# Kernel tuning notes

Measured on AMD Instinct MI355X. Metric: run time of the kernel, lower is better.

The kernel has to match this reference:

```python
import jax, jax.numpy as jnp
import numpy as np

FEAT = 1152
HID = [768, 512, 256]
WS = 32
LN_EPS = 1e-5


def _ln(x, g, b):
    mu = jnp.mean(x, axis=-1, keepdims=True)
    var = jnp.mean(jnp.square(x - mu), axis=-1, keepdims=True)
    return (x - mu) * jax.lax.rsqrt(var + LN_EPS) * g + b


def setup_inputs() -> dict:
    key = jax.random.key(0)
    ks = jax.random.split(key, 16)
    B, N, C = 8, 9216, FEAT

    def lin(k, din, dout):
        s = 1.0 / np.sqrt(din)
        k1, k2 = jax.random.split(k)
        return (jax.random.uniform(k1, (din, dout), jnp.float32, -s, s),
                jax.random.uniform(k2, (dout,), jnp.float32, -s, s))

    x = jax.random.normal(ks[0], (B, N, C), jnp.float32)
    W1, b1 = lin(ks[1], C, HID[0])
    W2, b2 = lin(ks[2], HID[0], HID[1])
    W3, b3 = lin(ks[3], HID[1], HID[2])
    Wo, bo = lin(ks[4], HID[2], C)
    red = C // 8
    ca_w1, ca_b1 = lin(ks[5], C, red)
    ca_w2, ca_b2 = lin(ks[6], red, C)
    return {
        "x": x,
        "W1": W1, "b1": b1, "g1": jnp.ones((HID[0],)), "be1": jnp.zeros((HID[0],)),
        "W2": W2, "b2": b2, "g2": jnp.ones((HID[1],)), "be2": jnp.zeros((HID[1],)),
        "W3": W3, "b3": b3, "g3": jnp.ones((HID[2],)), "be3": jnp.zeros((HID[2],)),
        "Wo": Wo, "bo": bo,
        "ca_w1": ca_w1, "ca_b1": ca_b1, "ca_w2": ca_w2, "ca_b2": ca_b2,
    }


def reference(x, W1, b1, g1, be1, W2, b2, g2, be2, W3, b3, g3, be3,
              Wo, bo, ca_w1, ca_b1, ca_w2, ca_b2):
    B, N, C = x.shape
    # projection + hidden blocks: Linear -> GELU(exact) -> LayerNorm
    h = _ln(jax.nn.gelu(x @ W1 + b1, approximate=False), g1, be1)
    h = _ln(jax.nn.gelu(h @ W2 + b2, approximate=False), g2, be2)
    h = _ln(jax.nn.gelu(h @ W3 + b3, approximate=False), g3, be3)
    y = h @ Wo + bo  # (B, N, C)
    # SE channel attention: global avg-pool over seq, 1x1 convs (=linear)
    pooled = jnp.mean(y, axis=1)                                  # (B, C)
    s = jax.nn.relu(pooled @ ca_w1 + ca_b1)                       # (B, C/8)
    s = jax.nn.sigmoid(s @ ca_w2 + ca_b2)                         # (B, C)
    y = y * s[:, None, :]
    # block-diagonal local self-attention, window = WS, scale 1/sqrt(C)
    nw = N // WS
    yw = y.reshape(B, nw, WS, C)
    scores = jnp.einsum('bwqc,bwkc->bwqk', yw, yw) / jnp.sqrt(jnp.asarray(C, y.dtype))
    attn = jax.nn.softmax(scores, axis=-1)
    out = jnp.einsum('bwqk,bwkc->bwqc', attn, yw)
    return out.reshape(B, N, C)
```

## Files before the change

kernel.cpp:

```cpp
#include <hip/hip_runtime.h>
#include <cstdint>
#include <cstddef>

typedef __bf16 bf16;
typedef __bf16 bf16x8 __attribute__((ext_vector_type(8)));
typedef float f32x4 __attribute__((ext_vector_type(4)));

__device__ __forceinline__ void gload_lds16(const bf16* g, bf16* l) {
    __builtin_amdgcn_global_load_lds((const __attribute__((address_space(1))) void*)g,
                                     (__attribute__((address_space(3))) void*)l, 16, 0, 0);
}

__global__ void cvt_f32_bf16_kernel(const float* __restrict__ in, bf16* __restrict__ outp, size_t n) {
    const size_t i = ((size_t)blockIdx.x * 256 + threadIdx.x) * 8;
    if (i >= n) return;
    const float4 a = *(const float4*)(in + i);
    const float4 b = *(const float4*)(in + i + 4);
    bf16x8 o;
    o[0] = (bf16)a.x; o[1] = (bf16)a.y; o[2] = (bf16)a.z; o[3] = (bf16)a.w;
    o[4] = (bf16)b.x; o[5] = (bf16)b.y; o[6] = (bf16)b.z; o[7] = (bf16)b.w;
    *(bf16x8*)(outp + i) = o;
}

__global__ void wtrans_kernel(const float* __restrict__ W, bf16* __restrict__ Wt, int K, int N) {
    const int idx = blockIdx.x * 256 + threadIdx.x;
    const int n = idx / K, k = idx - n * K;
    Wt[idx] = (bf16)W[(size_t)k * N + n];
}

__global__ void gemm_bf16_kernel(const bf16* __restrict__ A, const bf16* __restrict__ Bt,
                                 const float* __restrict__ bias, bf16* __restrict__ C,
                                 int K, int N, int do_gelu)
{
    __shared__ bf16 Alds[128 * 64];
    __shared__ bf16 Blds[128 * 64];
    const int t = threadIdx.x;
    const int w = t >> 6;
    const int l = t & 63;
    const int l15 = l & 15, l4 = l >> 4;
    const int m0 = blockIdx.y << 7;
    const int n0 = blockIdx.x << 7;
    const int wm = (w >> 1) << 6;
    const int wn = (w & 1) << 6;

    f32x4 acc[4][4] = {};

    int sr[4], sg[4];
#pragma unroll
    for (int i = 0; i < 4; ++i) {
        const int flat = i * 256 + t;
        sr[i] = flat >> 3;
        sg[i] = ((flat & 7) ^ (sr[i] & 7)) << 3;
    }

    for (int k0 = 0; k0 < K; k0 += 64) {
#pragma unroll
        for (int i = 0; i < 4; ++i) {
            gload_lds16(A + (size_t)(m0 + sr[i]) * K + (k0 + sg[i]),
                        &Alds[(size_t)(i * 256 + (w << 6)) << 3]);
            gload_lds16(Bt + (size_t)(n0 + sr[i]) * K + (k0 + sg[i]),
                        &Blds[(size_t)(i * 256 + (w << 6)) << 3]);
        }
        __syncthreads();
#pragma unroll
        for (int kk = 0; kk < 2; ++kk) {
            bf16x8 af[4], bfv[4];
#pragma unroll
            for (int i = 0; i < 4; ++i) {
                const int r = wm + (i << 4) + l15;
                const int g = (kk << 2) + l4;
                af[i] = *(const bf16x8*)&Alds[(r << 6) + ((g ^ (r & 7)) << 3)];
                const int rn = wn + (i << 4) + l15;
                bfv[i] = *(const bf16x8*)&Blds[(rn << 6) + ((g ^ (rn & 7)) << 3)];
            }
#pragma unroll
            for (int i = 0; i < 4; ++i)
#pragma unroll
                for (int j = 0; j < 4; ++j)
                    acc[i][j] = __builtin_amdgcn_mfma_f32_16x16x32_bf16(af[i], bfv[j], acc[i][j], 0, 0, 0);
        }
        __syncthreads();
    }

#pragma unroll
    for (int i = 0; i < 4; ++i) {
        const int mb = m0 + wm + (i << 4) + (l4 << 2);
#pragma unroll
        for (int j = 0; j < 4; ++j) {
            const int col = n0 + wn + (j << 4) + l15;
            const float bv = bias[col];
#pragma unroll
            for (int r = 0; r < 4; ++r) {
                float v = acc[i][j][r] + bv;
                if (do_gelu) v = 0.5f * v * (1.0f + erff(v * 0.70710678118654752f));
                C[(size_t)(mb + r) * N + col] = (bf16)v;
            }
        }
    }
}

template <int N>
__global__ void ln_kernel(bf16* __restrict__ H, const float* __restrict__ g,
                          const float* __restrict__ be)
{
    constexpr int NG = N / 8;
    const int t = threadIdx.x;
    bf16* hp = H + (size_t)blockIdx.x * N;
    float v[8];
    float s1 = 0.f, s2 = 0.f;
    if (t < NG) {
        const bf16x8 hv = *(const bf16x8*)(hp + t * 8);
#pragma unroll
        for (int e = 0; e < 8; ++e) { v[e] = (float)hv[e]; s1 += v[e]; s2 += v[e] * v[e]; }
    }
#pragma unroll
    for (int m = 1; m < 64; m <<= 1) { s1 += __shfl_xor(s1, m, 64); s2 += __shfl_xor(s2, m, 64); }
    __shared__ float red[4];
    const int w = t >> 6;
    if ((t & 63) == 0) { red[w] = s1; red[w + 2] = s2; }
    __syncthreads();
    s1 = red[0] + red[1];
    s2 = red[2] + red[3];
    const float mu = s1 * (1.0f / N);
    const float rstd = rsqrtf(s2 * (1.0f / N) - mu * mu + 1e-5f);
    if (t < NG) {
        const float4 g0 = *(const float4*)(g + t * 8);
        const float4 g1 = *(const float4*)(g + t * 8 + 4);
        const float4 b0 = *(const float4*)(be + t * 8);
        const float4 b1 = *(const float4*)(be + t * 8 + 4);
        bf16x8 o;
        o[0] = (bf16)((v[0] - mu) * rstd * g0.x + b0.x);
        o[1] = (bf16)((v[1] - mu) * rstd * g0.y + b0.y);
        o[2] = (bf16)((v[2] - mu) * rstd * g0.z + b0.z);
        o[3] = (bf16)((v[3] - mu) * rstd * g0.w + b0.w);
        o[4] = (bf16)((v[4] - mu) * rstd * g1.x + b1.x);
        o[5] = (bf16)((v[5] - mu) * rstd * g1.y + b1.y);
        o[6] = (bf16)((v[6] - mu) * rstd * g1.z + b1.z);
        o[7] = (bf16)((v[7] - mu) * rstd * g1.w + b1.w);
        *(bf16x8*)(hp + t * 8) = o;
    }
}

__global__ void pool1_kernel(const bf16* __restrict__ Y, float* __restrict__ ppart) {
    const int c = blockIdx.x * 128 + threadIdx.x;
    const int nc = blockIdx.y;
    const int b = blockIdx.z;
    const bf16* yp = Y + ((size_t)b * 9216 + (size_t)nc * 256) * 1152 + c;
    float s = 0.f;
#pragma unroll 4
    for (int i = 0; i < 256; ++i) s += (float)yp[(size_t)i * 1152];
    ppart[((size_t)b * 36 + nc) * 1152 + c] = s;
}

__global__ void pool2_kernel(const float* __restrict__ ppart, float* __restrict__ pooled) {
    const int i = blockIdx.x * 256 + threadIdx.x;
    const int b = i / 1152, c = i - b * 1152;
    float s = 0.f;
#pragma unroll
    for (int j = 0; j < 36; ++j) s += ppart[((size_t)b * 36 + j) * 1152 + c];
    pooled[i] = s;
}

__global__ void se_kernel(const float* __restrict__ pooled,
                          const float* __restrict__ w1, const float* __restrict__ b1,
                          const float* __restrict__ w2, const float* __restrict__ b2,
                          float* __restrict__ sbuf)
{
    const int b = blockIdx.x, t = threadIdx.x;
    __shared__ float p[1152];
    __shared__ float t1[144];
    for (int c = t; c < 1152; c += 256) p[c] = pooled[b * 1152 + c] * (1.0f / 9216.0f);
    __syncthreads();
    if (t < 144) {
        float a = b1[t];
        for (int k = 0; k < 1152; ++k) a += p[k] * w1[k * 144 + t];
        t1[t] = a > 0.f ? a : 0.f;
    }
    __syncthreads();
    for (int c = t; c < 1152; c += 256) {
        float a = b2[c];
#pragma unroll 8
        for (int k = 0; k < 144; ++k) a += t1[k] * w2[k * 1152 + c];
        sbuf[b * 1152 + c] = 1.0f / (1.0f + expf(-a));
    }
}

__global__ void attn_kernel(const bf16* __restrict__ Y, const float* __restrict__ sbuf,
                            float* __restrict__ out)
{
    __shared__ bf16 yw[32 * 384];
    __shared__ float Sp[4][32][33];
    __shared__ bf16 P[32 * 32];

    const int t = threadIdx.x;
    const int w = t >> 6, l = t & 63;
    const int l15 = l & 15, l4 = l >> 4;
    const int wdx = blockIdx.x, b = blockIdx.y;

    const bf16* Yp = Y + ((size_t)b * 9216 + (size_t)wdx * 32) * 1152;
    const float* sv = sbuf + b * 1152;
    float* op = out + ((size_t)b * 9216 + (size_t)wdx * 32) * 1152;

    auto stage_chunk = [&](int cc) {
#pragma unroll
        for (int i = 0; i < 6; ++i) {
            const int flat = i * 256 + t;
            const int r = flat / 48;
            const int gg = flat - r * 48;
            const int c0 = cc * 384 + gg * 8;
            const bf16x8 yv = *(const bf16x8*)(Yp + (size_t)r * 1152 + c0);
            const float4 sa = *(const float4*)(sv + c0);
            const float4 sb = *(const float4*)(sv + c0 + 4);
            bf16x8 ov;
            ov[0] = (bf16)((float)yv[0] * sa.x);
            ov[1] = (bf16)((float)yv[1] * sa.y);
            ov[2] = (bf16)((float)yv[2] * sa.z);
            ov[3] = (bf16)((float)yv[3] * sa.w);
            ov[4] = (bf16)((float)yv[4] * sb.x);
            ov[5] = (bf16)((float)yv[5] * sb.y);
            ov[6] = (bf16)((float)yv[6] * sb.z);
            ov[7] = (bf16)((float)yv[7] * sb.w);
            *(bf16x8*)&yw[((r * 48) + (gg ^ (r & 7))) << 3] = ov;
        }
    };

    f32x4 acc[2][2] = {};
    for (int cc = 0; cc < 3; ++cc) {
        if (cc) __syncthreads();
        stage_chunk(cc);
        __syncthreads();
#pragma unroll
        for (int kkl = 0; kkl < 3; ++kkl) {
            const int g = ((w * 3 + kkl) << 2) + l4;
            bf16x8 af[2];
#pragma unroll
            for (int i = 0; i < 2; ++i) {
                const int r = (i << 4) + l15;
                af[i] = *(const bf16x8*)&yw[((r * 48) + (g ^ (r & 7))) << 3];
            }
#pragma unroll
            for (int i = 0; i < 2; ++i)
#pragma unroll
                for (int j = 0; j < 2; ++j)
                    acc[i][j] = __builtin_amdgcn_mfma_f32_16x16x32_bf16(af[i], af[j], acc[i][j], 0, 0, 0);
        }
    }
#pragma unroll
    for (int i = 0; i < 2; ++i)
#pragma unroll
        for (int j = 0; j < 2; ++j)
#pragma unroll
            for (int r = 0; r < 4; ++r)
                Sp[w][(i << 4) + (l4 << 2) + r][(j << 4) + l15] = acc[i][j][r];
    __syncthreads();

    {
        const int q = t >> 3, u = t & 7;
        float v[4];
#pragma unroll
        for (int e = 0; e < 4; ++e) {
            const int k2 = (u << 2) + e;
            v[e] = (Sp[0][q][k2] + Sp[1][q][k2] + Sp[2][q][k2] + Sp[3][q][k2]) * 0.029462782549439483f;
        }
        float mx = fmaxf(fmaxf(v[0], v[1]), fmaxf(v[2], v[3]));
#pragma unroll
        for (int m = 1; m < 8; m <<= 1) mx = fmaxf(mx, __shfl_xor(mx, m, 64));
        float sm = 0.f;
#pragma unroll
        for (int e = 0; e < 4; ++e) { v[e] = expf(v[e] - mx); sm += v[e]; }
#pragma unroll
        for (int m = 1; m < 8; m <<= 1) sm += __shfl_xor(sm, m, 64);
        const float inv = 1.0f / sm;
#pragma unroll
        for (int e = 0; e < 4; ++e) P[(q << 5) + (u << 2) + e] = (bf16)(v[e] * inv);
    }
    __syncthreads();

    bf16x8 pa[2];
#pragma unroll
    for (int i = 0; i < 2; ++i)
        pa[i] = *(const bf16x8*)&P[(((i << 4) + l15) << 5) + (l4 << 3)];

    for (int ci = 0; ci < 3; ++ci) {
        const int cc = (ci == 0) ? 2 : (ci - 1);
        if (ci) {
            __syncthreads();
            stage_chunk(cc);
            __syncthreads();
        }
        f32x4 pacc[2][6] = {};
#pragma unroll
        for (int jn = 0; jn < 6; ++jn) {
            const int nl = w * 96 + (jn << 4) + l15;
            const int gg = nl >> 3, e = nl & 7;
            bf16x8 bv;
#pragma unroll
            for (int j = 0; j < 8; ++j) {
                const int kr = (l4 << 3) + j;
                bv[j] = yw[(((kr * 48) + (gg ^ (kr & 7))) << 3) + e];
            }
#pragma unroll
            for (int i = 0; i < 2; ++i)
                pacc[i][jn] = __builtin_amdgcn_mfma_f32_16x16x32_bf16(pa[i], bv, pacc[i][jn], 0, 0, 0);
        }
#pragma unroll
        for (int i = 0; i < 2; ++i) {
            const int mb = (i << 4) + (l4 << 2);
#pragma unroll
            for (int jn = 0; jn < 6; ++jn) {
                const int cg = cc * 384 + w * 96 + (jn << 4) + l15;
#pragma unroll
                for (int r = 0; r < 4; ++r)
                    op[(size_t)(mb + r) * 1152 + cg] = pacc[i][jn][r];
            }
        }
    }
}

extern "C" void kernel_launch(void* const* d_in, const int* in_sizes, int n_in,
                              void* d_out, int out_size, void* d_ws, size_t ws_size,
                              hipStream_t stream)
{
    const float* x   = (const float*)d_in[0];
    const float* W1  = (const float*)d_in[1];
    const float* b1  = (const float*)d_in[2];
    const float* g1  = (const float*)d_in[3];
    const float* be1 = (const float*)d_in[4];
    const float* W2  = (const float*)d_in[5];
    const float* b2  = (const float*)d_in[6];
    const float* g2  = (const float*)d_in[7];
    const float* be2 = (const float*)d_in[8];
    const float* W3  = (const float*)d_in[9];
    const float* b3  = (const float*)d_in[10];
    const float* g3  = (const float*)d_in[11];
    const float* be3 = (const float*)d_in[12];
    const float* Wo  = (const float*)d_in[13];
    const float* bo  = (const float*)d_in[14];
    const float* cw1 = (const float*)d_in[15];
    const float* cb1 = (const float*)d_in[16];
    const float* cw2 = (const float*)d_in[17];
    const float* cb2 = (const float*)d_in[18];
    float* out = (float*)d_out;

    const int M = 8 * 9216;
    size_t off = 0;
    auto alloc = [&](size_t nbytes) {
        void* p = (char*)d_ws + off;
        off += (nbytes + 255) & ~(size_t)255;
        return p;
    };
    bf16* Xb  = (bf16*)alloc((size_t)M * 1152 * 2);
    bf16* Hb  = (bf16*)alloc((size_t)M * 768 * 2);
    bf16* H2  = (bf16*)alloc((size_t)M * 512 * 2);
    bf16* Wt1 = (bf16*)alloc(768ull * 1152 * 2);
    bf16* Wt2 = (bf16*)alloc(512ull * 768 * 2);
    bf16* Wt3 = (bf16*)alloc(256ull * 512 * 2);
    bf16* Wto = (bf16*)alloc(1152ull * 256 * 2);
    float* ppart  = (float*)alloc(8ull * 36 * 1152 * 4);
    float* pooled = (float*)alloc(8ull * 1152 * 4);
    float* sbuf   = (float*)alloc(8ull * 1152 * 4);
    bf16* H1 = Hb;
    bf16* H3 = Hb;
    bf16* Y  = Xb;

    cvt_f32_bf16_kernel<<<41472, 256, 0, stream>>>(x, Xb, (size_t)M * 1152);
    wtrans_kernel<<<3456, 256, 0, stream>>>(W1, Wt1, 1152, 768);
    wtrans_kernel<<<1536, 256, 0, stream>>>(W2, Wt2, 768, 512);
    wtrans_kernel<<<512,  256, 0, stream>>>(W3, Wt3, 512, 256);
    wtrans_kernel<<<1152, 256, 0, stream>>>(Wo, Wto, 256, 1152);

    gemm_bf16_kernel<<<dim3(6, 576), 256, 0, stream>>>(Xb, Wt1, b1, H1, 1152, 768, 1);
    ln_kernel<768><<<M, 128, 0, stream>>>(H1, g1, be1);
    gemm_bf16_kernel<<<dim3(4, 576), 256, 0, stream>>>(H1, Wt2, b2, H2, 768, 512, 1);
    ln_kernel<512><<<M, 128, 0, stream>>>(H2, g2, be2);
    gemm_bf16_kernel<<<dim3(2, 576), 256, 0, stream>>>(H2, Wt3, b3, H3, 512, 256, 1);
    ln_kernel<256><<<M, 128, 0, stream>>>(H3, g3, be3);
    gemm_bf16_kernel<<<dim3(9, 576), 256, 0, stream>>>(H3, Wto, bo, Y, 256, 1152, 0);

    pool1_kernel<<<dim3(9, 36, 8), 128, 0, stream>>>(Y, ppart);
    pool2_kernel<<<36, 256, 0, stream>>>(ppart, pooled);
    se_kernel<<<8, 256, 0, stream>>>(pooled, cw1, cb1, cw2, cb2, sbuf);
    attn_kernel<<<dim3(288, 8), 256, 0, stream>>>(Y, sbuf, out);
}
```

Before: 922.3 us.

## Fuse fp32-to-bf16 input conversion into first GEMM, swizzle blocks across XCDs, pack LN rows

Removes the standalone fp32→bf16 conversion pass over the input. The first GEMM now loads fp32 tiles of x straight into LDS and converts them to bf16 while building MFMA fragments, which avoids a full write and re-read of a large intermediate. The GEMM grids become 1-D with an XCD-aware block swizzle to improve L2 locality. The LayerNorm kernels now put several rows in each block to cut the number of launched blocks and idle threads. In exchange, the first GEMM uses twice the LDS for its A tile and does the conversion inside its inner loop.

```diff
diff --git a/kernel.cpp b/kernel.cpp
--- a/kernel.cpp
+++ b/kernel.cpp
@@ -10,16 +10,9 @@
     __builtin_amdgcn_global_load_lds((const __attribute__((address_space(1))) void*)g,
                                      (__attribute__((address_space(3))) void*)l, 16, 0, 0);
 }
-
-__global__ void cvt_f32_bf16_kernel(const float* __restrict__ in, bf16* __restrict__ outp, size_t n) {
-    const size_t i = ((size_t)blockIdx.x * 256 + threadIdx.x) * 8;
-    if (i >= n) return;
-    const float4 a = *(const float4*)(in + i);
-    const float4 b = *(const float4*)(in + i + 4);
-    bf16x8 o;
-    o[0] = (bf16)a.x; o[1] = (bf16)a.y; o[2] = (bf16)a.z; o[3] = (bf16)a.w;
-    o[4] = (bf16)b.x; o[5] = (bf16)b.y; o[6] = (bf16)b.z; o[7] = (bf16)b.w;
-    *(bf16x8*)(outp + i) = o;
+__device__ __forceinline__ void gload_lds16f(const float* g, float* l) {
+    __builtin_amdgcn_global_load_lds((const __attribute__((address_space(1))) void*)g,
+                                     (__attribute__((address_space(3))) void*)l, 16, 0, 0);
 }
 
 __global__ void wtrans_kernel(const float* __restrict__ W, bf16* __restrict__ Wt, int K, int N) {
@@ -28,9 +21,13 @@
     Wt[idx] = (bf16)W[(size_t)k * N + n];
 }
 
+__device__ __forceinline__ int xcd_swz(int bid, int nwg) {
+    return (bid & 7) * (nwg >> 3) + (bid >> 3);
+}
+
 __global__ void gemm_bf16_kernel(const bf16* __restrict__ A, const bf16* __restrict__ Bt,
                                  const float* __restrict__ bias, bf16* __restrict__ C,
-                                 int K, int N, int do_gelu)
+                                 int K, int N, int nx, int do_gelu)
 {
     __shared__ bf16 Alds[128 * 64];
     __shared__ bf16 Blds[128 * 64];
@@ -38,8 +35,11 @@
     const int w = t >> 6;
     const int l = t & 63;
     const int l15 = l & 15, l4 = l >> 4;
-    const int m0 = blockIdx.y << 7;
-    const int n0 = blockIdx.x << 7;
+    const int wgid = xcd_swz(blockIdx.x, gridDim.x);
+    const int mblk = wgid / nx;
+    const int nblk = wgid - mblk * nx;
+    const int m0 = mblk << 7;
+    const int n0 = nblk << 7;
     const int wm = (w >> 1) << 6;
     const int wn = (w & 1) << 6;
 
@@ -99,35 +99,124 @@
     }
 }
 
-template <int N>
-__global__ void ln_kernel(bf16* __restrict__ H, const float* __restrict__ g,
-                          const float* __restrict__ be)
-{
-    constexpr int NG = N / 8;
+__global__ void gemm_f32a_kernel(const float* __restrict__ A, const bf16* __restrict__ Bt,
+                                 const float* __restrict__ bias, bf16* __restrict__ C,
+                                 int K, int N, int nx)
+{
+    __shared__ float Af32[128 * 64];
+    __shared__ bf16  Blds[128 * 64];
     const int t = threadIdx.x;
-    bf16* hp = H + (size_t)blockIdx.x * N;
+    const int w = t >> 6;
+    const int l = t & 63;
+    const int l15 = l & 15, l4 = l >> 4;
+    const int wgid = xcd_swz(blockIdx.x, gridDim.x);
+    const int mblk = wgid / nx;
+    const int nblk = wgid - mblk * nx;
+    const int m0 = mblk << 7;
+    const int n0 = nblk << 7;
+    const int wm = (w >> 1) << 6;
+    const int wn = (w & 1) << 6;
+
+    f32x4 acc[4][4] = {};
+
+    int ar[8], ag[8];
+#pragma unroll
+    for (int i = 0; i < 8; ++i) {
+        const int flat = i * 256 + t;
+        ar[i] = flat >> 4;
+        ag[i] = ((flat & 15) ^ (ar[i] & 7)) << 2;
+    }
+    int br[4], bg[4];
+#pragma unroll
+    for (int i = 0; i < 4; ++i) {
+        const int flat = i * 256 + t;
+        br[i] = flat >> 3;
+        bg[i] = ((flat & 7) ^ (br[i] & 7)) << 3;
+    }
+
+    for (int k0 = 0; k0 < K; k0 += 64) {
+#pragma unroll
+        for (int i = 0; i < 8; ++i)
+            gload_lds16f(A + (size_t)(m0 + ar[i]) * K + (k0 + ag[i]),
+                         &Af32[(size_t)(i * 256 + (w << 6)) << 2]);
+#pragma unroll
+        for (int i = 0; i < 4; ++i)
+            gload_lds16(Bt + (size_t)(n0 + br[i]) * K + (k0 + bg[i]),
+                        &Blds[(size_t)(i * 256 + (w << 6)) << 3]);
+        __syncthreads();
+#pragma unroll
+        for (int kk = 0; kk < 2; ++kk) {
+            bf16x8 af[4], bfv[4];
+#pragma unroll
+            for (int i = 0; i < 4; ++i) {
+                const int r = wm + (i << 4) + l15;
+                const int fg = (kk << 3) + (l4 << 1);
+                const float4 fa = *(const float4*)&Af32[(r << 6) + ((fg ^ (r & 7)) << 2)];
+                const float4 fb = *(const float4*)&Af32[(r << 6) + (((fg + 1) ^ (r & 7)) << 2)];
+                bf16x8 a;
+                a[0] = (bf16)fa.x; a[1] = (bf16)fa.y; a[2] = (bf16)fa.z; a[3] = (bf16)fa.w;
+                a[4] = (bf16)fb.x; a[5] = (bf16)fb.y; a[6] = (bf16)fb.z; a[7] = (bf16)fb.w;
+                af[i] = a;
+                const int rn = wn + (i << 4) + l15;
+                const int g = (kk << 2) + l4;
+                bfv[i] = *(const bf16x8*)&Blds[(rn << 6) + ((g ^ (rn & 7)) << 3)];
+            }
+#pragma unroll
+            for (int i = 0; i < 4; ++i)
+#pragma unroll
+                for (int j = 0; j < 4; ++j)
+                    acc[i][j] = __builtin_amdgcn_mfma_f32_16x16x32_bf16(af[i], bfv[j], acc[i][j], 0, 0, 0);
+        }
+        __syncthreads();
+    }
+
+#pragma unroll
+    for (int i = 0; i < 4; ++i) {
+        const int mb = m0 + wm + (i << 4) + (l4 << 2);
+#pragma unroll
+        for (int j = 0; j < 4; ++j) {
+            const int col = n0 + wn + (j << 4) + l15;
+            const float bv = bias[col];
+#pragma unroll
+            for (int r = 0; r < 4; ++r) {
+                float v = acc[i][j][r] + bv;
+                v = 0.5f * v * (1.0f + erff(v * 0.70710678118654752f));
+                C[(size_t)(mb + r) * N + col] = (bf16)v;
+            }
+        }
+    }
+}
+
+__global__ void ln768_kernel(bf16* __restrict__ H, const float* __restrict__ g,
+                             const float* __restrict__ be)
+{
+    const int t = threadIdx.x;
+    const int rloc = t >> 7;
+    const int u = t & 127;
+    bf16* hp = H + ((size_t)blockIdx.x * 2 + rloc) * 768;
     float v[8];
     float s1 = 0.f, s2 = 0.f;
-    if (t < NG) {
-        const bf16x8 hv = *(const bf16x8*)(hp + t * 8);
+    if (u < 96) {
+        const bf16x8 hv = *(const bf16x8*)(hp + u * 8);
 #pragma unroll
         for (int e = 0; e < 8; ++e) { v[e] = (float)hv[e]; s1 += v[e]; s2 += v[e] * v[e]; }
     }
 #pragma unroll
     for (int m = 1; m < 64; m <<= 1) { s1 += __shfl_xor(s1, m, 64); s2 += __shfl_xor(s2, m, 64); }
-    __shared__ float red[4];
+    __shared__ float red[8];
     const int w = t >> 6;
-    if ((t & 63) == 0) { red[w] = s1; red[w + 2] = s2; }
+    if ((t & 63) == 0) { red[w] = s1; red[w + 4] = s2; }
     __syncthreads();
-    s1 = red[0] + red[1];
-    s2 = red[2] + red[3];
-    const float mu = s1 * (1.0f / N);
-    const float rstd = rsqrtf(s2 * (1.0f / N) - mu * mu + 1e-5f);
-    if (t < NG) {
-        const float4 g0 = *(const float4*)(g + t * 8);
-        const float4 g1 = *(const float4*)(g + t * 8 + 4);
-        const float4 b0 = *(const float4*)(be + t * 8);
-        const float4 b1 = *(const float4*)(be + t * 8 + 4);
+    const int wb = rloc << 1;
+    s1 = red[wb] + red[wb + 1];
+    s2 = red[wb + 4] + red[wb + 5];
+    const float mu = s1 * (1.0f / 768.0f);
+    const float rstd = rsqrtf(s2 * (1.0f / 768.0f) - mu * mu + 1e-5f);
+    if (u < 96) {
+        const float4 g0 = *(const float4*)(g + u * 8);
+        const float4 g1 = *(const float4*)(g + u * 8 + 4);
+        const float4 b0 = *(const float4*)(be + u * 8);
+        const float4 b1 = *(const float4*)(be + u * 8 + 4);
         bf16x8 o;
         o[0] = (bf16)((v[0] - mu) * rstd * g0.x + b0.x);
         o[1] = (bf16)((v[1] - mu) * rstd * g0.y + b0.y);
@@ -137,8 +226,70 @@
         o[5] = (bf16)((v[5] - mu) * rstd * g1.y + b1.y);
         o[6] = (bf16)((v[6] - mu) * rstd * g1.z + b1.z);
         o[7] = (bf16)((v[7] - mu) * rstd * g1.w + b1.w);
-        *(bf16x8*)(hp + t * 8) = o;
-    }
+        *(bf16x8*)(hp + u * 8) = o;
+    }
+}
+
+__global__ void ln512_kernel(bf16* __restrict__ H, const float* __restrict__ g,
+                             const float* __restrict__ be)
+{
+    const int t = threadIdx.x;
+    const int w = t >> 6, l = t & 63;
+    bf16* hp = H + ((size_t)blockIdx.x * 4 + w) * 512;
+    const bf16x8 hv = *(const bf16x8*)(hp + l * 8);
+    float v[8];
+    float s1 = 0.f, s2 = 0.f;
+#pragma unroll
+    for (int e = 0; e < 8; ++e) { v[e] = (float)hv[e]; s1 += v[e]; s2 += v[e] * v[e]; }
+#pragma unroll
+    for (int m = 1; m < 64; m <<= 1) { s1 += __shfl_xor(s1, m, 64); s2 += __shfl_xor(s2, m, 64); }
+    const float mu = s1 * (1.0f / 512.0f);
+    const float rstd = rsqrtf(s2 * (1.0f / 512.0f) - mu * mu + 1e-5f);
+    const float4 g0 = *(const float4*)(g + l * 8);
+    const float4 g1 = *(const float4*)(g + l * 8 + 4);
+    const float4 b0 = *(const float4*)(be + l * 8);
+    const float4 b1 = *(const float4*)(be + l * 8 + 4);
+    bf16x8 o;
+    o[0] = (bf16)((v[0] - mu) * rstd * g0.x + b0.x);
+    o[1] = (bf16)((v[1] - mu) * rstd * g0.y + b0.y);
+    o[2] = (bf16)((v[2] - mu) * rstd * g0.z + b0.z);
+    o[3] = (bf16)((v[3] - mu) * rstd * g0.w + b0.w);
+    o[4] = (bf16)((v[4] - mu) * rstd * g1.x + b1.x);
+    o[5] = (bf16)((v[5] - mu) * rstd * g1.y + b1.y);
+    o[6] = (bf16)((v[6] - mu) * rstd * g1.z + b1.z);
+    o[7] = (bf16)((v[7] - mu) * rstd * g1.w + b1.w);
+    *(bf16x8*)(hp + l * 8) = o;
+}
+
+__global__ void ln256_kernel(bf16* __restrict__ H, const float* __restrict__ g,
+                             const float* __restrict__ be)
+{
+    const int t = threadIdx.x;
+    const int rloc = t >> 5, l = t & 31;
+    bf16* hp = H + ((size_t)blockIdx.x * 8 + rloc) * 256;
+    const bf16x8 hv = *(const bf16x8*)(hp + l * 8);
+    float v[8];
+    float s1 = 0.f, s2 = 0.f;
+#pragma unroll
+    for (int e = 0; e < 8; ++e) { v[e] = (float)hv[e]; s1 += v[e]; s2 += v[e] * v[e]; }
+#pragma unroll
+    for (int m = 1; m < 32; m <<= 1) { s1 += __shfl_xor(s1, m, 64); s2 += __shfl_xor(s2, m, 64); }
+    const float mu = s1 * (1.0f / 256.0f);
+    const float rstd = rsqrtf(s2 * (1.0f / 256.0f) - mu * mu + 1e-5f);
+    const float4 g0 = *(const float4*)(g + l * 8);
+    const float4 g1 = *(const float4*)(g + l * 8 + 4);
+    const float4 b0 = *(const float4*)(be + l * 8);
+    const float4 b1 = *(const float4*)(be + l * 8 + 4);
+    bf16x8 o;
+    o[0] = (bf16)((v[0] - mu) * rstd * g0.x + b0.x);
+    o[1] = (bf16)((v[1] - mu) * rstd * g0.y + b0.y);
+    o[2] = (bf16)((v[2] - mu) * rstd * g0.z + b0.z);
+    o[3] = (bf16)((v[3] - mu) * rstd * g0.w + b0.w);
+    o[4] = (bf16)((v[4] - mu) * rstd * g1.x + b1.x);
+    o[5] = (bf16)((v[5] - mu) * rstd * g1.y + b1.y);
+    o[6] = (bf16)((v[6] - mu) * rstd * g1.z + b1.z);
+    o[7] = (bf16)((v[7] - mu) * rstd * g1.w + b1.w);
+    *(bf16x8*)(hp + l * 8) = o;
 }
 
 __global__ void pool1_kernel(const bf16* __restrict__ Y, float* __restrict__ ppart) {
@@ -349,7 +500,7 @@
         off += (nbytes + 255) & ~(size_t)255;
         return p;
     };
-    bf16* Xb  = (bf16*)alloc((size_t)M * 1152 * 2);
+    bf16* Yb  = (bf16*)alloc((size_t)M * 1152 * 2);
     bf16* Hb  = (bf16*)alloc((size_t)M * 768 * 2);
     bf16* H2  = (bf16*)alloc((size_t)M * 512 * 2);
     bf16* Wt1 = (bf16*)alloc(768ull * 1152 * 2);
@@ -361,24 +512,22 @@
     float* sbuf   = (float*)alloc(8ull * 1152 * 4);
     bf16* H1 = Hb;
     bf16* H3 = Hb;
-    bf16* Y  = Xb;
-
-    cvt_f32_bf16_kernel<<<41472, 256, 0, stream>>>(x, Xb, (size_t)M * 1152);
+
     wtrans_kernel<<<3456, 256, 0, stream>>>(W1, Wt1, 1152, 768);
     wtrans_kernel<<<1536, 256, 0, stream>>>(W2, Wt2, 768, 512);
     wtrans_kernel<<<512,  256, 0, stream>>>(W3, Wt3, 512, 256);
     wtrans_kernel<<<1152, 256, 0, stream>>>(Wo, Wto, 256, 1152);
 
-    gemm_bf16_kernel<<<dim3(6, 576), 256, 0, stream>>>(Xb, Wt1, b1, H1, 1152, 768, 1);
-    ln_kernel<768><<<M, 128, 0, stream>>>(H1, g1, be1);
-    gemm_bf16_kernel<<<dim3(4, 576), 256, 0, stream>>>(H1, Wt2, b2, H2, 768, 512, 1);
-    ln_kernel<512><<<M, 128, 0, stream>>>(H2, g2, be2);
-    gemm_bf16_kernel<<<dim3(2, 576), 256, 0, stream>>>(H2, Wt3, b3, H3, 512, 256, 1);
-    ln_kernel<256><<<M, 128, 0, stream>>>(H3, g3, be3);
-    gemm_bf16_kernel<<<dim3(9, 576), 256, 0, stream>>>(H3, Wto, bo, Y, 256, 1152, 0);
-
-    pool1_kernel<<<dim3(9, 36, 8), 128, 0, stream>>>(Y, ppart);
+    gemm_f32a_kernel<<<6 * 576, 256, 0, stream>>>(x, Wt1, b1, H1, 1152, 768, 6);
+    ln768_kernel<<<M / 2, 256, 0, stream>>>(H1, g1, be1);
+    gemm_bf16_kernel<<<4 * 576, 256, 0, stream>>>(H1, Wt2, b2, H2, 768, 512, 4, 1);
+    ln512_kernel<<<M / 4, 256, 0, stream>>>(H2, g2, be2);
+    gemm_bf16_kernel<<<2 * 576, 256, 0, stream>>>(H2, Wt3, b3, H3, 512, 256, 2, 1);
+    ln256_kernel<<<M / 8, 256, 0, stream>>>(H3, g3, be3);
+    gemm_bf16_kernel<<<9 * 576, 256, 0, stream>>>(H3, Wto, bo, Yb, 256, 1152, 9, 0);
+
+    pool1_kernel<<<dim3(9, 36, 8), 128, 0, stream>>>(Yb, ppart);
     pool2_kernel<<<36, 256, 0, stream>>>(ppart, pooled);
     se_kernel<<<8, 256, 0, stream>>>(pooled, cw1, cb1, cw2, cb2, sbuf);
-    attn_kernel<<<dim3(288, 8), 256, 0, stream>>>(Y, sbuf, out);
-}
+    attn_kernel<<<dim3(288, 8), 256, 0, stream>>>(Yb, sbuf, out);
+}
```

After: 869.7 us. 5.7% less time.
